# Kernel optimization log

Hardware: AMD Instinct MI355X
Metric: run time of the kernel (lower is better)

## Reference

```python
import jax, jax.numpy as jnp
import numpy as np

K = 9  # 3x3 kernel field

def _conv(x, w, b, pad):
    out = jax.lax.conv_general_dilated(x, w, (1, 1), ((pad, pad), (pad, pad)),
                                       dimension_numbers=('NCHW', 'OIHW', 'NCHW'))
    return out + b[None, :, None, None]

def _conv_transpose(x, w, b):
    # torch ConvTranspose2d(k=3, stride=2, padding=1, output_padding=1); w: [Cin, Cout, 3, 3]
    wk = jnp.flip(jnp.transpose(w, (1, 0, 2, 3)), axis=(2, 3))  # [Cout, Cin, 3, 3]
    out = jax.lax.conv_general_dilated(x, wk, (1, 1), ((1, 2), (1, 2)),
                                       lhs_dilation=(2, 2),
                                       dimension_numbers=('NCHW', 'OIHW', 'NCHW'))
    return out + b[None, :, None, None]

def _modulated_deform_conv(x, offset, mask, w, b):
    # x: [B,C,H,W], offset: [B,2K,H,W] (y,x interleaved per kernel point, row-major),
    # mask: [B,K,H,W], w: [O,C,3,3]; stride=1, pad=1, dilation=1
    B, C, H, W = x.shape
    O = w.shape[0]
    off = offset.reshape(B, K, 2, H, W)
    ky, kx = jnp.meshgrid(jnp.arange(3), jnp.arange(3), indexing='ij')
    base_y = (jnp.arange(H)[None, :, None] - 1 + ky.reshape(K, 1, 1)).astype(x.dtype)  # [K,H,1]
    base_x = (jnp.arange(W)[None, None, :] - 1 + kx.reshape(K, 1, 1)).astype(x.dtype)  # [K,1,W]
    py = off[:, :, 0] + base_y[None]  # [B,K,H,W]
    px = off[:, :, 1] + base_x[None]
    y0 = jnp.floor(py); x0 = jnp.floor(px)
    wy = py - y0; wx = px - x0
    y0i = y0.astype(jnp.int32); x0i = x0.astype(jnp.int32)
    flat = x.reshape(B, C, H * W)

    def gather(yi, xi):
        valid = ((yi >= 0) & (yi < H) & (xi >= 0) & (xi < W)).astype(x.dtype)
        idx = jnp.clip(yi, 0, H - 1) * W + jnp.clip(xi, 0, W - 1)  # [B,K,H,W]
        g = jax.vmap(lambda im, ix: im[:, ix])(flat, idx.reshape(B, -1))  # [B,C,K*H*W]
        return g.reshape(B, C, K, H, W) * valid[:, None]

    v = (gather(y0i, x0i)         * ((1 - wy) * (1 - wx))[:, None]
       + gather(y0i, x0i + 1)     * ((1 - wy) * wx)[:, None]
       + gather(y0i + 1, x0i)     * (wy * (1 - wx))[:, None]
       + gather(y0i + 1, x0i + 1) * (wy * wx)[:, None])
    v = v * mask[:, None]  # modulation
    out = jnp.einsum('bckhw,ock->bohw', v, w.reshape(O, C, K))
    return out + b[None, :, None, None]

def setup_inputs() -> dict:
    key = jax.random.key(0)
    ks = jax.random.split(key, 8)
    B, Cin, Cout, H, W = 4, 128, 64, 64, 64
    return {
        'high_feature': jax.random.normal(ks[0], (B, Cin, H, W), jnp.float32),
        'low_feature': jax.random.normal(ks[1], (B, Cout, 2 * H, 2 * W), jnp.float32),
        'w_up': jax.random.normal(ks[2], (Cin, Cout, 3, 3), jnp.float32) * 0.03,
        'b_up': jnp.zeros((Cout,), jnp.float32),
        'w_off': jax.random.normal(ks[3], (3 * K, 2 * Cout, 3, 3), jnp.float32) * 0.02,
        'b_off': jnp.zeros((3 * K,), jnp.float32),
        'w_align': jax.random.normal(ks[4], (Cout, Cout, 3, 3), jnp.float32) * 0.04,
        'b_align': jnp.zeros((Cout,), jnp.float32),
    }

def reference(high_feature, low_feature, w_up, b_up, w_off, b_off, w_align, b_align):
    up = _conv_transpose(high_feature, w_up, b_up)            # [B,Cout,2H,2W]
    fo = _conv(jnp.concatenate([up, low_feature], axis=1), w_off, b_off, 1)
    offset, mask = fo[:, :2 * K], fo[:, 2 * K:]
    mask = 2.0 * jax.nn.sigmoid(mask)
    aligned = _modulated_deform_conv(up, offset, mask, w_align, b_align)
    aligned = jnp.where(aligned >= 0, aligned, 0.2 * aligned)  # LeakyReLU(0.2)
    return jnp.concatenate([aligned, low_feature], axis=1)
```

## Files before the change

kernel.cpp:

```cpp
#include <hip/hip_runtime.h>
#include <math.h>

namespace {
constexpr int B   = 4;
constexpr int CIN = 128;
constexpr int CO  = 64;
constexpr int HF  = 64;
constexpr int HO  = 128;
constexpr int HW  = HO * HO;
constexpr int NOFF = 27;

constexpr size_t UPB  = 0;
constexpr size_t LOB  = UPB + (size_t)B * HW * CO / 2;
constexpr size_t HBF  = LOB + (size_t)B * HW * CO / 2;
constexpr size_t WFRG = HBF + (size_t)B * HF * HF * CIN / 2;
constexpr size_t WFUP = WFRG + (size_t)(4 * 18 * 64 * 8) / 2;
constexpr size_t WFOF = WFUP + (size_t)(9 * 4 * 4 * 64 * 8) / 2;
}

using short8 = __attribute__((ext_vector_type(8))) short;
using f32x4  = __attribute__((ext_vector_type(4))) float;

__device__ __forceinline__ unsigned short f2bf(float f) {
  unsigned u = __float_as_uint(f);
  u += 0x7fffu + ((u >> 16) & 1u);
  return (unsigned short)(u >> 16);
}

__global__ __launch_bounds__(256) void k_prep(const float* __restrict__ high,
                                              const float* __restrict__ wup,
                                              const float* __restrict__ woff,
                                              const float* __restrict__ wal,
                                              float* __restrict__ ws) {
  __shared__ unsigned short tl2[32][66];
  const int bid = blockIdx.x;
  const int t = threadIdx.x;

  if (bid < 288) {
    int i = bid * 256 + t;
    if (i < 4 * 18 * 64 * 8) {
      int j = i & 7; int t2 = i >> 3;
      int lane = t2 & 63; int t3 = t2 >> 6;
      int kb = t3 % 18; int w = t3 / 18;
      int tap = kb >> 1;
      int c = (kb & 1) * 32 + ((lane >> 4) << 3) + j;
      int o = (w << 4) + (lane & 15);
      unsigned short* wfrag = (unsigned short*)(ws + WFRG);
      wfrag[i] = f2bf(wal[((size_t)o * CO + c) * 9 + tap]);
    }
    if (i < 9 * 4 * 4 * 64 * 8) {
      int j = i & 7; int lane = (i >> 3) & 63; int w = (i >> 9) & 3;
      int ch = (i >> 11) & 3; int rr = i >> 13;
      int c = ch * 32 + ((lane >> 4) << 3) + j;
      int o = w * 16 + (lane & 15);
      unsigned short* wfup = (unsigned short*)(ws + WFUP);
      wfup[i] = f2bf(wup[((size_t)c * CO + o) * 9 + rr]);
    }
    if (i < 9 * 4 * 2 * 64 * 8) {
      int j = i & 7; int lane = (i >> 3) & 63; int nt = (i >> 9) & 1;
      int kc = (i >> 10) & 3; int tap = i >> 12;
      int c = kc * 32 + ((lane >> 4) << 3) + j;
      int o = nt * 16 + (lane & 15);
      float v = 0.f;
      if (o < NOFF) v = woff[(((size_t)o * 2 * CO + c) * 3 + tap / 3) * 3 + (tap % 3)];
      unsigned short* wfo = (unsigned short*)(ws + WFOF);
      wfo[i] = f2bf(v);
    }
    return;
  }

  {
    unsigned short* hbf = (unsigned short*)(ws + HBF);
    int j = bid - 288;
    const int y = j & 63, b = j >> 6;
    const int x = t & 63, clb = t >> 6;
    for (int c0 = 0; c0 < CIN; c0 += 32) {
      __syncthreads();
#pragma unroll
      for (int k = 0; k < 8; ++k) {
        int cl = clb * 8 + k;
        float v = high[(((size_t)b * CIN + c0 + cl) * HF + y) * HF + x];
        tl2[cl][x] = f2bf(v);
      }
      __syncthreads();
      int px = t >> 2, cg = t & 3;
      ushort4 a, bb;
      a.x = tl2[cg * 8 + 0][px]; a.y = tl2[cg * 8 + 1][px];
      a.z = tl2[cg * 8 + 2][px]; a.w = tl2[cg * 8 + 3][px];
      bb.x = tl2[cg * 8 + 4][px]; bb.y = tl2[cg * 8 + 5][px];
      bb.z = tl2[cg * 8 + 6][px]; bb.w = tl2[cg * 8 + 7][px];
      unsigned short* dst = hbf + (((size_t)b * HF + y) * HF + px) * CIN + c0 + cg * 8;
      *(ushort4*)(dst) = a;
      *(ushort4*)(dst + 4) = bb;
    }
  }
}

union SmemUp {
  unsigned short At[2][4][85][8];
  float accs[4][16][65];
  unsigned short tl[64][130];
};

__global__ __launch_bounds__(256) void k_up(const float* __restrict__ low,
                                            const float* __restrict__ bup,
                                            float* __restrict__ out,
                                            float* __restrict__ ws) {
  __shared__ SmemUp sm;
  const int t = threadIdx.x;

  if (blockIdx.x >= 1024) {
    unsigned short* lob = (unsigned short*)(ws + LOB);
    int j = blockIdx.x - 1024;
    const int y = j & 127, b = j >> 7;
#pragma unroll
    for (int it = 0; it < 8; ++it) {
      int i = it * 256 + t;
      int c = i >> 5, xi = (i & 31) * 4;
      float4 v = *(const float4*)(low + (((size_t)b * CO + c) * HO + y) * HO + xi);
      *(float4*)(out + (((size_t)b * 2 * CO + CO + c) * HO + y) * HO + xi) = v;
      sm.tl[c][xi + 0] = f2bf(v.x); sm.tl[c][xi + 1] = f2bf(v.y);
      sm.tl[c][xi + 2] = f2bf(v.z); sm.tl[c][xi + 3] = f2bf(v.w);
    }
    __syncthreads();
#pragma unroll
    for (int it = 0; it < 4; ++it) {
      int i = it * 256 + t;
      int x = i >> 3, cg = i & 7;
      unsigned rw[4];
#pragma unroll
      for (int p = 0; p < 4; ++p)
        rw[p] = (unsigned)sm.tl[cg * 8 + 2 * p][x] | ((unsigned)sm.tl[cg * 8 + 2 * p + 1][x] << 16);
      *(uint4*)(lob + (((size_t)b * HO + y) * HO + x) * CO + cg * 8) =
          make_uint4(rw[0], rw[1], rw[2], rw[3]);
    }
    return;
  }

  const unsigned short* hbf = (const unsigned short*)(ws + HBF);
  const uint4* wfu = (const uint4*)(ws + WFUP);
  unsigned short* upb = (unsigned short*)(ws + UPB);

  const int lane = t & 63;
  const int oq   = __builtin_amdgcn_readfirstlane(t >> 6);
  const int orig = blockIdx.x;
  const int tile = ((orig & 7) << 7) + (orig >> 3);
  const int par  = tile & 3;
  const int pyv  = (par >> 1) & 1, pxv = par & 1;
  const int tx   = ((tile >> 2) & 3) * 16;
  const int ty   = ((tile >> 4) & 15) * 4;
  const int b    = tile >> 8;
  const int nty  = pyv + 1, ntx = pxv + 1;

  uint4 s0, s1;
  const int pxA = t >> 2, cgA = t & 3;
  const int i2 = t + 256, pxB = i2 >> 2, cgB = i2 & 3;

  auto load_chunk = [&](int c0) {
    {
      int gy = ty + pxA / 17, gx = tx + pxA % 17;
      s0 = make_uint4(0, 0, 0, 0);
      if (gy < HF && gx < HF)
        s0 = *(const uint4*)(hbf + (((size_t)b * HF + gy) * HF + gx) * CIN + c0 + cgA * 8);
    }
    s1 = make_uint4(0, 0, 0, 0);
    if (pxB < 85) {
      int gy = ty + pxB / 17, gx = tx + pxB % 17;
      if (gy < HF && gx < HF)
        s1 = *(const uint4*)(hbf + (((size_t)b * HF + gy) * HF + gx) * CIN + c0 + cgB * 8);
    }
  };
  auto write_chunk = [&](int buf) {
    *(uint4*)&sm.At[buf][cgA][pxA][0] = s0;
    if (pxB < 85) *(uint4*)&sm.At[buf][cgB][pxB][0] = s1;
  };

  f32x4 acc[4];
#pragma unroll
  for (int mt = 0; mt < 4; ++mt) acc[mt] = {0.f, 0.f, 0.f, 0.f};

  load_chunk(0);
  write_chunk(0);
  __syncthreads();

  union Cvt { uint4 u; short8 s; };
  int buf = 0;
#pragma unroll 1
  for (int ch = 0; ch < 4; ++ch) {
    if (ch < 3) load_chunk((ch + 1) * 32);
#pragma unroll
    for (int ti = 0; ti < 2; ++ti) {
      if (ti < nty) {
#pragma unroll
        for (int tj = 0; tj < 2; ++tj) {
          if (tj < ntx) {
            int ryA = pyv ? 2 - 2 * ti : 1;
            int rxA = pxv ? 2 - 2 * tj : 1;
            int rr = ryA * 3 + rxA;
            Cvt bw; bw.u = wfu[(((size_t)rr * 4 + ch) * 4 + oq) * 64 + lane];
#pragma unroll
            for (int mt = 0; mt < 4; ++mt) {
              Cvt av;
              av.u = *(const uint4*)&sm.At[buf][lane >> 4][(mt + ti) * 17 + (lane & 15) + tj][0];
              acc[mt] = __builtin_amdgcn_mfma_f32_16x16x32_bf16(av.s, bw.s, acc[mt], 0, 0, 0);
            }
          }
        }
      }
    }
    if (ch < 3) write_chunk(buf ^ 1);
    __syncthreads();
    buf ^= 1;
  }

#pragma unroll
  for (int mt = 0; mt < 4; ++mt)
#pragma unroll
    for (int r = 0; r < 4; ++r)
      sm.accs[oq][lane & 15][mt * 16 + (lane >> 4) * 4 + r] = acc[mt][r];
  __syncthreads();

  const int yo = 2 * (ty + (lane >> 4)) + pyv;
  const int xo = 2 * (tx + (lane & 15)) + pxv;
  unsigned short* dst = upb + (((size_t)b * HO + yo) * HO + xo) * CO + oq * 16;
  unsigned rw[8];
#pragma unroll
  for (int p = 0; p < 8; ++p) {
    float v0 = sm.accs[oq][2 * p][lane] + bup[oq * 16 + 2 * p];
    float v1 = sm.accs[oq][2 * p + 1][lane] + bup[oq * 16 + 2 * p + 1];
    rw[p] = (unsigned)f2bf(v0) | ((unsigned)f2bf(v1) << 16);
  }
  *(uint4*)dst = make_uint4(rw[0], rw[1], rw[2], rw[3]);
  *(uint4*)(dst + 8) = make_uint4(rw[4], rw[5], rw[6], rw[7]);
}

__global__ __launch_bounds__(256) void k_offdcn(const float* __restrict__ boff,
                                                const float* __restrict__ bal,
                                                float* __restrict__ out,
                                                const float* __restrict__ ws) {
  __shared__ float smem[7936];
  unsigned short* us_in = (unsigned short*)smem;
  float* fo_raw = smem;
  unsigned* prm = (unsigned*)(smem + 2112);
  unsigned short* us_vt = (unsigned short*)(smem + 3840);

  const unsigned short* upb = (const unsigned short*)(ws + UPB);
  const unsigned short* lob = (const unsigned short*)(ws + LOB);
  const uint4* wfo = (const uint4*)(ws + WFOF);
  const uint4* wf  = (const uint4*)(ws + WFRG);

  const int t = threadIdx.x;
  const int lane = t & 63;
  const int w = __builtin_amdgcn_readfirstlane(t >> 6);
  const int mh = w >> 1, nt = w & 1;
  const int oq = w;
  const int orig = blockIdx.x;
  const int tile = ((orig & 7) << 7) + (orig >> 3);
  const int tX = (tile & 7) * 16;
  const int tY = ((tile >> 3) & 31) * 4;
  const int b  = tile >> 8;
  const unsigned short* upB = upb + (size_t)b * HW * CO;

  union Cvt { uint4 u; short8 s; };

  for (int i = t; i < 16 * 108; i += 256) {
    int px = i >> 4, cg = i & 15;
    int gy = tY - 1 + px / 18, gx = tX - 1 + px % 18;
    uint4 v = make_uint4(0, 0, 0, 0);
    if (gy >= 0 && gy < HO && gx >= 0 && gx < HO) {
      const unsigned short* src =
          (cg < 8 ? upb : lob) + (((size_t)b * HO + gy) * HO + gx) * CO + (cg & 7) * 8;
      v = *(const uint4*)src;
    }
    *(uint4*)&us_in[((size_t)cg * 108 + px) * 8] = v;
  }
  __syncthreads();

  f32x4 acc2[2];
  acc2[0] = {0.f, 0.f, 0.f, 0.f}; acc2[1] = {0.f, 0.f, 0.f, 0.f};
#pragma unroll 1
  for (int tap = 0; tap < 9; ++tap) {
    int ky = tap / 3, kx = tap % 3;
#pragma unroll
    for (int kc = 0; kc < 4; ++kc) {
      Cvt bw; bw.u = wfo[(((size_t)tap * 4 + kc) * 2 + nt) * 64 + lane];
#pragma unroll
      for (int mt = 0; mt < 2; ++mt) {
        int sy = mh * 2 + mt;
        Cvt av;
        av.u = *(const uint4*)&us_in[(((size_t)(kc * 4 + (lane >> 4))) * 108 +
                                      (sy + ky) * 18 + (lane & 15) + kx) * 8];
        acc2[mt] = __builtin_amdgcn_mfma_f32_16x16x32_bf16(av.s, bw.s, acc2[mt], 0, 0, 0);
      }
    }
  }
  __syncthreads();

#pragma unroll
  for (int mt = 0; mt < 2; ++mt)
#pragma unroll
    for (int r = 0; r < 4; ++r)
      fo_raw[(nt * 16 + (lane & 15)) * 66 + mh * 32 + mt * 16 + (lane >> 4) * 4 + r] =
          acc2[mt][r];
  __syncthreads();

  for (int i = t; i < 9 * 64; i += 256) {
    int k = i >> 6, px = i & 63;
    int y = tY + (px >> 4), x = tX + (px & 15);
    float offy = fo_raw[(2 * k) * 66 + px] + boff[2 * k];
    float offx = fo_raw[(2 * k + 1) * 66 + px] + boff[2 * k + 1];
    float m = 2.f / (1.f + expf(-(fo_raw[(18 + k) * 66 + px] + boff[18 + k])));
    float pyf = offy + (float)(y - 1 + k / 3);
    float pxf = offx + (float)(x - 1 + k % 3);
    float y0f = floorf(pyf), x0f = floorf(pxf);
    float wy = pyf - y0f, wx = pxf - x0f;
    int y0 = (int)y0f, x0 = (int)x0f;
    int y1 = y0 + 1, x1 = x0 + 1;
    float vy0 = (y0 >= 0 && y0 < HO) ? m : 0.f;
    float vy1 = (y1 >= 0 && y1 < HO) ? m : 0.f;
    float vx0 = (x0 >= 0 && x0 < HO) ? 1.f : 0.f;
    float vx1 = (x1 >= 0 && x1 < HO) ? 1.f : 0.f;
    float w0 = (1.f - wy) * (1.f - wx) * vy0 * vx0;
    float w1 = (1.f - wy) * wx * vy0 * vx1;
    float w2 = wy * (1.f - wx) * vy1 * vx0;
    float w3 = wy * wx * vy1 * vx1;
    int cy0 = min(max(y0, 0), HO - 1), cy1 = min(max(y1, 0), HO - 1);
    int cx0 = min(max(x0, 0), HO - 1), cx1 = min(max(x1, 0), HO - 1);
    unsigned pc = (unsigned)cy0 | ((unsigned)cy1 << 8) |
                  ((unsigned)cx0 << 16) | ((unsigned)cx1 << 24);
    unsigned* pr = prm + ((size_t)k * 64 + px) * 3;
    pr[0] = (unsigned)f2bf(w0) | ((unsigned)f2bf(w1) << 16);
    pr[1] = (unsigned)f2bf(w2) | ((unsigned)f2bf(w3) << 16);
    pr[2] = pc;
  }
  __syncthreads();

  uint4 u00[2], u01[2], u10[2], u11[2];

  auto issue = [&](int k) {
#pragma unroll
    for (int it = 0; it < 2; ++it) {
      int j = it * 256 + t;
      int q = j & 7, px = j >> 3;
      unsigned pc = prm[((size_t)k * 64 + px) * 3 + 2];
      int cy0 = pc & 255, cy1 = (pc >> 8) & 255, cx0 = (pc >> 16) & 255, cx1 = pc >> 24;
      const unsigned short* base = upB + q * 8;
      u00[it] = *(const uint4*)(base + (size_t)(cy0 * HO + cx0) * CO);
      u01[it] = *(const uint4*)(base + (size_t)(cy0 * HO + cx1) * CO);
      u10[it] = *(const uint4*)(base + (size_t)(cy1 * HO + cx0) * CO);
      u11[it] = *(const uint4*)(base + (size_t)(cy1 * HO + cx1) * CO);
    }
  };

  auto combine = [&](int k, int buf) {
#pragma unroll
    for (int it = 0; it < 2; ++it) {
      int j = it * 256 + t;
      int q = j & 7, px = j >> 3;
      const unsigned* pr = prm + ((size_t)k * 64 + px) * 3;
      unsigned pw01 = pr[0], pw23 = pr[1];
      float w0 = __uint_as_float(pw01 << 16), w1 = __uint_as_float(pw01 & 0xffff0000u);
      float w2 = __uint_as_float(pw23 << 16), w3 = __uint_as_float(pw23 & 0xffff0000u);
      unsigned a0[4] = {u00[it].x, u00[it].y, u00[it].z, u00[it].w};
      unsigned a1[4] = {u01[it].x, u01[it].y, u01[it].z, u01[it].w};
      unsigned a2[4] = {u10[it].x, u10[it].y, u10[it].z, u10[it].w};
      unsigned a3[4] = {u11[it].x, u11[it].y, u11[it].z, u11[it].w};
      unsigned rw[4];
#pragma unroll
      for (int p = 0; p < 4; ++p) {
        float l0 = __uint_as_float(a0[p] << 16), h0 = __uint_as_float(a0[p] & 0xffff0000u);
        float l1 = __uint_as_float(a1[p] << 16), h1 = __uint_as_float(a1[p] & 0xffff0000u);
        float l2 = __uint_as_float(a2[p] << 16), h2 = __uint_as_float(a2[p] & 0xffff0000u);
        float l3 = __uint_as_float(a3[p] << 16), h3 = __uint_as_float(a3[p] & 0xffff0000u);
        float vlo = fmaf(w0, l0, fmaf(w1, l1, fmaf(w2, l2, w3 * l3)));
        float vhi = fmaf(w0, h0, fmaf(w1, h1, fmaf(w2, h2, w3 * h3)));
        rw[p] = (unsigned)f2bf(vlo) | ((unsigned)f2bf(vhi) << 16);
      }
      *(uint4*)&us_vt[(((size_t)buf * 8 + q) * 64 + px) * 8] = make_uint4(rw[0], rw[1], rw[2], rw[3]);
    }
  };

  f32x4 acc[4];
#pragma unroll
  for (int mt = 0; mt < 4; ++mt) acc[mt] = {0.f, 0.f, 0.f, 0.f};

  uint4 bw0 = wf[(oq * 18 + 0) * 64 + lane];
  uint4 bw1 = wf[(oq * 18 + 1) * 64 + lane];
  uint4 bn0, bn1;

  issue(0);
  combine(0, 0);
  issue(1);
  __syncthreads();

  int buf = 0;
#pragma unroll 1
  for (int k = 0; k < 9; ++k) {
#pragma unroll
    for (int kb2 = 0; kb2 < 2; ++kb2) {
      Cvt bfr; bfr.u = kb2 ? bw1 : bw0;
#pragma unroll
      for (int mt = 0; mt < 4; ++mt) {
        Cvt av;
        av.u = *(const uint4*)&us_vt[(((size_t)buf * 8 + kb2 * 4 + (lane >> 4)) * 64 +
                                      mt * 16 + (lane & 15)) * 8];
        acc[mt] = __builtin_amdgcn_mfma_f32_16x16x32_bf16(av.s, bfr.s, acc[mt], 0, 0, 0);
      }
    }
    if (k < 8) {
      combine(k + 1, buf ^ 1);
      if (k < 7) issue(k + 2);
      bn0 = wf[(oq * 18 + 2 * k + 2) * 64 + lane];
      bn1 = wf[(oq * 18 + 2 * k + 3) * 64 + lane];
    }
    __syncthreads();
    bw0 = bn0; bw1 = bn1;
    buf ^= 1;
  }

  float* accs = smem;
#pragma unroll
  for (int mt = 0; mt < 4; ++mt)
#pragma unroll
    for (int r = 0; r < 4; ++r)
      accs[((size_t)oq * 16 + (lane & 15)) * 65 + mt * 16 + (lane >> 4) * 4 + r] = acc[mt][r];
  __syncthreads();

  const int y = tY + (lane >> 4), x = tX + (lane & 15);
  float* ob = out + (size_t)b * 2 * CO * HW + (size_t)y * HO + x;
#pragma unroll
  for (int ol = 0; ol < 16; ++ol) {
    int o = oq * 16 + ol;
    float v = accs[((size_t)oq * 16 + ol) * 65 + lane] + bal[o];
    v = (v >= 0.f) ? v : 0.2f * v;
    ob[(size_t)o * HW] = v;
  }
}

extern "C" void kernel_launch(void* const* d_in, const int* in_sizes, int n_in,
                              void* d_out, int out_size, void* d_ws, size_t ws_size,
                              hipStream_t stream) {
  const float* high = (const float*)d_in[0];
  const float* low  = (const float*)d_in[1];
  const float* wup  = (const float*)d_in[2];
  const float* bup  = (const float*)d_in[3];
  const float* woff = (const float*)d_in[4];
  const float* boff = (const float*)d_in[5];
  const float* wal  = (const float*)d_in[6];
  const float* bal  = (const float*)d_in[7];
  float* out = (float*)d_out;
  float* ws  = (float*)d_ws;

  k_prep<<<dim3(544), dim3(256), 0, stream>>>(high, wup, woff, wal, ws);
  k_up<<<dim3(1536), dim3(256), 0, stream>>>(low, bup, out, ws);
  k_offdcn<<<dim3(1024), dim3(256), 0, stream>>>(boff, bal, out, ws);
}
```

Baseline: 61.77 us.

## Switch intermediate storage and MFMA from bf16 to fp16 with packed-half bilinear combine

All intermediate activations and weight fragments are now stored as fp16 instead of bf16, and the MFMA calls use the f16 variant. The bilinear sampling combine in the deformable-conv kernel now works on packed half2 FMAs instead of unpacking to fp32. Bilinear weights are stored as duplicated half2 pairs, which enlarges the shared-memory parameter area. The aim is to cut ALU work for conversions and the combine step. In exchange, the narrower fp16 range can overflow, and accumulating the interpolation in half precision loses accuracy.

```diff
diff --git a/kernel.cpp b/kernel.cpp
--- a/kernel.cpp
+++ b/kernel.cpp
@@ -18,14 +18,18 @@
 constexpr size_t WFOF = WFUP + (size_t)(9 * 4 * 4 * 64 * 8) / 2;
 }
 
-using short8 = __attribute__((ext_vector_type(8))) short;
-using f32x4  = __attribute__((ext_vector_type(4))) float;
-
-__device__ __forceinline__ unsigned short f2bf(float f) {
-  unsigned u = __float_as_uint(f);
-  u += 0x7fffu + ((u >> 16) & 1u);
-  return (unsigned short)(u >> 16);
-}
+using half8 = __attribute__((ext_vector_type(8))) _Float16;
+using h2    = __attribute__((ext_vector_type(2))) _Float16;
+using f32x4 = __attribute__((ext_vector_type(4))) float;
+
+__device__ __forceinline__ unsigned short f2h16(float f) {
+  return __builtin_bit_cast(unsigned short, (_Float16)f);
+}
+__device__ __forceinline__ unsigned pkh(float a, float b) {
+  return __builtin_bit_cast(unsigned, __builtin_amdgcn_cvt_pkrtz(a, b));
+}
+__device__ __forceinline__ h2 u2h(unsigned u) { return __builtin_bit_cast(h2, u); }
+__device__ __forceinline__ unsigned h2u(h2 v) { return __builtin_bit_cast(unsigned, v); }
 
 __global__ __launch_bounds__(256) void k_prep(const float* __restrict__ high,
                                               const float* __restrict__ wup,
@@ -46,7 +50,7 @@
       int c = (kb & 1) * 32 + ((lane >> 4) << 3) + j;
       int o = (w << 4) + (lane & 15);
       unsigned short* wfrag = (unsigned short*)(ws + WFRG);
-      wfrag[i] = f2bf(wal[((size_t)o * CO + c) * 9 + tap]);
+      wfrag[i] = f2h16(wal[((size_t)o * CO + c) * 9 + tap]);
     }
     if (i < 9 * 4 * 4 * 64 * 8) {
       int j = i & 7; int lane = (i >> 3) & 63; int w = (i >> 9) & 3;
@@ -54,7 +58,7 @@
       int c = ch * 32 + ((lane >> 4) << 3) + j;
       int o = w * 16 + (lane & 15);
       unsigned short* wfup = (unsigned short*)(ws + WFUP);
-      wfup[i] = f2bf(wup[((size_t)c * CO + o) * 9 + rr]);
+      wfup[i] = f2h16(wup[((size_t)c * CO + o) * 9 + rr]);
     }
     if (i < 9 * 4 * 2 * 64 * 8) {
       int j = i & 7; int lane = (i >> 3) & 63; int nt = (i >> 9) & 1;
@@ -64,7 +68,7 @@
       float v = 0.f;
       if (o < NOFF) v = woff[(((size_t)o * 2 * CO + c) * 3 + tap / 3) * 3 + (tap % 3)];
       unsigned short* wfo = (unsigned short*)(ws + WFOF);
-      wfo[i] = f2bf(v);
+      wfo[i] = f2h16(v);
     }
     return;
   }
@@ -80,7 +84,7 @@
       for (int k = 0; k < 8; ++k) {
         int cl = clb * 8 + k;
         float v = high[(((size_t)b * CIN + c0 + cl) * HF + y) * HF + x];
-        tl2[cl][x] = f2bf(v);
+        tl2[cl][x] = f2h16(v);
       }
       __syncthreads();
       int px = t >> 2, cg = t & 3;
@@ -119,8 +123,8 @@
       int c = i >> 5, xi = (i & 31) * 4;
       float4 v = *(const float4*)(low + (((size_t)b * CO + c) * HO + y) * HO + xi);
       *(float4*)(out + (((size_t)b * 2 * CO + CO + c) * HO + y) * HO + xi) = v;
-      sm.tl[c][xi + 0] = f2bf(v.x); sm.tl[c][xi + 1] = f2bf(v.y);
-      sm.tl[c][xi + 2] = f2bf(v.z); sm.tl[c][xi + 3] = f2bf(v.w);
+      sm.tl[c][xi + 0] = f2h16(v.x); sm.tl[c][xi + 1] = f2h16(v.y);
+      sm.tl[c][xi + 2] = f2h16(v.z); sm.tl[c][xi + 3] = f2h16(v.w);
     }
     __syncthreads();
 #pragma unroll
@@ -183,7 +187,7 @@
   write_chunk(0);
   __syncthreads();
 
-  union Cvt { uint4 u; short8 s; };
+  union Cvt { uint4 u; half8 h; };
   int buf = 0;
 #pragma unroll 1
   for (int ch = 0; ch < 4; ++ch) {
@@ -202,7 +206,7 @@
             for (int mt = 0; mt < 4; ++mt) {
               Cvt av;
               av.u = *(const uint4*)&sm.At[buf][lane >> 4][(mt + ti) * 17 + (lane & 15) + tj][0];
-              acc[mt] = __builtin_amdgcn_mfma_f32_16x16x32_bf16(av.s, bw.s, acc[mt], 0, 0, 0);
+              acc[mt] = __builtin_amdgcn_mfma_f32_16x16x32_f16(av.h, bw.h, acc[mt], 0, 0, 0);
             }
           }
         }
@@ -228,7 +232,7 @@
   for (int p = 0; p < 8; ++p) {
     float v0 = sm.accs[oq][2 * p][lane] + bup[oq * 16 + 2 * p];
     float v1 = sm.accs[oq][2 * p + 1][lane] + bup[oq * 16 + 2 * p + 1];
-    rw[p] = (unsigned)f2bf(v0) | ((unsigned)f2bf(v1) << 16);
+    rw[p] = pkh(v0, v1);
   }
   *(uint4*)dst = make_uint4(rw[0], rw[1], rw[2], rw[3]);
   *(uint4*)(dst + 8) = make_uint4(rw[4], rw[5], rw[6], rw[7]);
@@ -238,11 +242,11 @@
                                                 const float* __restrict__ bal,
                                                 float* __restrict__ out,
                                                 const float* __restrict__ ws) {
-  __shared__ float smem[7936];
+  __shared__ float smem[9088];
   unsigned short* us_in = (unsigned short*)smem;
   float* fo_raw = smem;
   unsigned* prm = (unsigned*)(smem + 2112);
-  unsigned short* us_vt = (unsigned short*)(smem + 3840);
+  unsigned short* us_vt = (unsigned short*)(smem + 4992);
 
   const unsigned short* upb = (const unsigned short*)(ws + UPB);
   const unsigned short* lob = (const unsigned short*)(ws + LOB);
@@ -261,7 +265,7 @@
   const int b  = tile >> 8;
   const unsigned short* upB = upb + (size_t)b * HW * CO;
 
-  union Cvt { uint4 u; short8 s; };
+  union Cvt { uint4 u; half8 h; };
 
   for (int i = t; i < 16 * 108; i += 256) {
     int px = i >> 4, cg = i & 15;
@@ -290,7 +294,7 @@
         Cvt av;
         av.u = *(const uint4*)&us_in[(((size_t)(kc * 4 + (lane >> 4))) * 108 +
                                       (sy + ky) * 18 + (lane & 15) + kx) * 8];
-        acc2[mt] = __builtin_amdgcn_mfma_f32_16x16x32_bf16(av.s, bw.s, acc2[mt], 0, 0, 0);
+        acc2[mt] = __builtin_amdgcn_mfma_f32_16x16x32_f16(av.h, bw.h, acc2[mt], 0, 0, 0);
       }
     }
   }
@@ -328,10 +332,12 @@
     int cx0 = min(max(x0, 0), HO - 1), cx1 = min(max(x1, 0), HO - 1);
     unsigned pc = (unsigned)cy0 | ((unsigned)cy1 << 8) |
                   ((unsigned)cx0 << 16) | ((unsigned)cx1 << 24);
-    unsigned* pr = prm + ((size_t)k * 64 + px) * 3;
-    pr[0] = (unsigned)f2bf(w0) | ((unsigned)f2bf(w1) << 16);
-    pr[1] = (unsigned)f2bf(w2) | ((unsigned)f2bf(w3) << 16);
-    pr[2] = pc;
+    unsigned* pr = prm + ((size_t)k * 64 + px) * 5;
+    pr[0] = pkh(w0, w0);
+    pr[1] = pkh(w1, w1);
+    pr[2] = pkh(w2, w2);
+    pr[3] = pkh(w3, w3);
+    pr[4] = pc;
   }
   __syncthreads();
 
@@ -342,7 +348,7 @@
     for (int it = 0; it < 2; ++it) {
       int j = it * 256 + t;
       int q = j & 7, px = j >> 3;
-      unsigned pc = prm[((size_t)k * 64 + px) * 3 + 2];
+      unsigned pc = prm[((size_t)k * 64 + px) * 5 + 4];
       int cy0 = pc & 255, cy1 = (pc >> 8) & 255, cx0 = (pc >> 16) & 255, cx1 = pc >> 24;
       const unsigned short* base = upB + q * 8;
       u00[it] = *(const uint4*)(base + (size_t)(cy0 * HO + cx0) * CO);
@@ -357,10 +363,8 @@
     for (int it = 0; it < 2; ++it) {
       int j = it * 256 + t;
       int q = j & 7, px = j >> 3;
-      const unsigned* pr = prm + ((size_t)k * 64 + px) * 3;
-      unsigned pw01 = pr[0], pw23 = pr[1];
-      float w0 = __uint_as_float(pw01 << 16), w1 = __uint_as_float(pw01 & 0xffff0000u);
-      float w2 = __uint_as_float(pw23 << 16), w3 = __uint_as_float(pw23 & 0xffff0000u);
+      const unsigned* pr = prm + ((size_t)k * 64 + px) * 5;
+      h2 w0 = u2h(pr[0]), w1 = u2h(pr[1]), w2 = u2h(pr[2]), w3 = u2h(pr[3]);
       unsigned a0[4] = {u00[it].x, u00[it].y, u00[it].z, u00[it].w};
       unsigned a1[4] = {u01[it].x, u01[it].y, u01[it].z, u01[it].w};
       unsigned a2[4] = {u10[it].x, u10[it].y, u10[it].z, u10[it].w};
@@ -368,13 +372,11 @@
       unsigned rw[4];
 #pragma unroll
       for (int p = 0; p < 4; ++p) {
-        float l0 = __uint_as_float(a0[p] << 16), h0 = __uint_as_float(a0[p] & 0xffff0000u);
-        float l1 = __uint_as_float(a1[p] << 16), h1 = __uint_as_float(a1[p] & 0xffff0000u);
-        float l2 = __uint_as_float(a2[p] << 16), h2 = __uint_as_float(a2[p] & 0xffff0000u);
-        float l3 = __uint_as_float(a3[p] << 16), h3 = __uint_as_float(a3[p] & 0xffff0000u);
-        float vlo = fmaf(w0, l0, fmaf(w1, l1, fmaf(w2, l2, w3 * l3)));
-        float vhi = fmaf(w0, h0, fmaf(w1, h1, fmaf(w2, h2, w3 * h3)));
-        rw[p] = (unsigned)f2bf(vlo) | ((unsigned)f2bf(vhi) << 16);
+        h2 r = w3 * u2h(a3[p]);
+        r = __builtin_elementwise_fma(w2, u2h(a2[p]), r);
+        r = __builtin_elementwise_fma(w1, u2h(a1[p]), r);
+        r = __builtin_elementwise_fma(w0, u2h(a0[p]), r);
+        rw[p] = h2u(r);
       }
       *(uint4*)&us_vt[(((size_t)buf * 8 + q) * 64 + px) * 8] = make_uint4(rw[0], rw[1], rw[2], rw[3]);
     }
@@ -404,7 +406,7 @@
         Cvt av;
         av.u = *(const uint4*)&us_vt[(((size_t)buf * 8 + kb2 * 4 + (lane >> 4)) * 64 +
                                       mt * 16 + (lane & 15)) * 8];
-        acc[mt] = __builtin_amdgcn_mfma_f32_16x16x32_bf16(av.s, bfr.s, acc[mt], 0, 0, 0);
+        acc[mt] = __builtin_amdgcn_mfma_f32_16x16x32_f16(av.h, bfr.h, acc[mt], 0, 0, 0);
       }
     }
     if (k < 8) {
```

After: 58.08 us. -6.0%, faster.
